# Kernel optimization log

Hardware: AMD Instinct MI355X
Metric: run time of the kernel (lower is better)

The kernel has to match this reference:

```python
import jax, jax.numpy as jnp
import numpy as np

EPSILON = 0.05
MAX_ITER = 50
ALPHA = 6.0
THRESHOLD = 0.25
SCALE = 0.02  # keeps OT costs near THRESHOLD so the gate is not saturated


def setup_inputs() -> dict:
    key = jax.random.key(0)
    k1, k2 = jax.random.split(key)
    B, E, D, P = 8192, 8, 512, 32
    tokens = jax.random.normal(k1, (B, E, D), dtype=jnp.float32) * SCALE
    prototypes = jax.random.normal(k2, (E, P, D), dtype=jnp.float32) * SCALE
    return {"tokens": tokens, "prototypes": prototypes, "full_index": 0}


def _sinkhorn_log(cost, epsilon, max_iter):
    # cost: [..., n_source, n_target]; batched log-domain Sinkhorn, fixed iterations
    ns, nt = cost.shape[-2], cost.shape[-1]
    log_mu = jnp.full(cost.shape[:-1], -float(np.log(ns)), dtype=cost.dtype)
    log_nu = jnp.full(cost.shape[:-2] + (nt,), -float(np.log(nt)), dtype=cost.dtype)
    log_k = -cost / epsilon

    def step(carry, _):
        log_u, log_v = carry
        log_u = log_mu - jax.scipy.special.logsumexp(log_k + log_v[..., None, :], axis=-1)
        log_v = log_nu - jax.scipy.special.logsumexp(log_k + log_u[..., :, None], axis=-2)
        return (log_u, log_v), None

    (log_u, log_v), _ = jax.lax.scan(
        step, (jnp.zeros_like(log_mu), jnp.zeros_like(log_nu)), None, length=max_iter
    )
    return jnp.exp(log_k + log_u[..., :, None] + log_v[..., None, :])


def reference(tokens, prototypes, full_index):
    # tokens: [B, E, D], prototypes: [E, P, D]
    B, E, D = tokens.shape
    anchor = tokens[:, full_index, :]                                   # [B, D]
    source = jnp.stack(
        [tokens, jnp.broadcast_to(anchor[:, None, :], tokens.shape)], axis=2
    )                                                                   # [B, E, 2, D]
    # squared euclidean cdist: ||s||^2 - 2 s.p + ||p||^2
    s2 = jnp.sum(source * source, axis=-1)                              # [B, E, 2]
    p2 = jnp.sum(prototypes * prototypes, axis=-1)                      # [E, P]
    cross = jnp.einsum('besd,epd->besp', source, prototypes)            # [B, E, 2, P]
    cost = jnp.maximum(s2[..., None] - 2.0 * cross + p2[None, :, None, :], 0.0)
    transport = _sinkhorn_log(cost, EPSILON, MAX_ITER)                  # [B, E, 2, P]
    ot_cost = jnp.sum(transport * cost, axis=(-1, -2))                  # [B, E]
    validity = jax.nn.sigmoid(-ALPHA * (ot_cost - THRESHOLD))[..., None]  # [B, E, 1]
    # the full_index expert always passes with validity 1 and zero cost
    is_full = jnp.arange(E) == full_index                               # [E]
    ot_cost = jnp.where(is_full[None, :], 0.0, ot_cost)
    validity = jnp.where(is_full[None, :, None], 1.0, validity)
    return validity, ot_cost
```

## Files before the change

kernel.cpp:

```cpp
#include <hip/hip_runtime.h>
#include <hip/hip_bf16.h>


#define EXP2F(x) __builtin_amdgcn_exp2f(x)
#define LOG2F(x) __builtin_amdgcn_logf(x)
#define RCPF(x)  __builtin_amdgcn_rcpf(x)

typedef __bf16 bf16x8 __attribute__((ext_vector_type(8)));
typedef float  f32x4  __attribute__((ext_vector_type(4)));

#define BDIM 8192
#define EDIM 8
#define DDIM 512
#define PDIM 32
#define BPB  64
#define MROWS 128
#define NTHR 256
#define CSTRIDE 36
#define C_SCALE 28.853900817779268f
#define LOG2E   1.4426950408889634f

__device__ __forceinline__ bf16x8 cvt2(float4 a, float4 b) {
  bf16x8 r;
  r[0] = (__bf16)a.x; r[1] = (__bf16)a.y; r[2] = (__bf16)a.z; r[3] = (__bf16)a.w;
  r[4] = (__bf16)b.x; r[5] = (__bf16)b.y; r[6] = (__bf16)b.z; r[7] = (__bf16)b.w;
  return r;
}

__global__ __launch_bounds__(NTHR, 3)
void ot_noise_gate_kernel(const float* __restrict__ tokens,
                          const float* __restrict__ protos,
                          const int*   __restrict__ fullIndexPtr,
                          float*       __restrict__ out) {
  const int fi    = fullIndexPtr[0];
  const int e     = blockIdx.x & (EDIM - 1);
  const int chunk = blockIdx.x >> 3;
  const int b0    = chunk * BPB;
  float* outVal = out;
  float* outOt  = out + BDIM * EDIM;

  if (e == fi) {
    int t = threadIdx.x;
    if (t < BPB) {
      int b = b0 + t;
      outVal[b * EDIM + e] = 1.0f;
      outOt [b * EDIM + e] = 0.0f;
    }
    return;
  }

  __shared__ __align__(16) __bf16 sB[64 * PDIM * 8];
  __shared__ __align__(16) unsigned char sACraw[MROWS * CSTRIDE * 4];
  __shared__ float sNorm[MROWS];
  __shared__ float sPNp[8][33];
  __shared__ float sPN[PDIM];
  __bf16* sA = (__bf16*)sACraw;
  float*  sC = (float*)sACraw;

  const int t   = threadIdx.x;
  const int l   = t & 63;
  const int w   = t >> 6;
  const int fr  = l & 15;
  const int q4  = l >> 4;

  const int row = t >> 1;
  const int h   = t & 1;
  const float4* rowPtr = (const float4*)(tokens +
      ((size_t)(b0 + (row & 63)) * EDIM + ((row < 64) ? e : fi)) * DDIM);

  float4 pf[8];
  #pragma unroll
  for (int i2 = 0; i2 < 8; ++i2) pf[i2] = rowPtr[h * 8 + i2];

  {
    const float4* pG4 = (const float4*)(protos + (size_t)e * PDIM * DDIM);
    const int p  = t & 31;
    const int oh = t >> 5;
    float pnp = 0.f;
    #pragma unroll
    for (int pass = 0; pass < 8; ++pass) {
      int oct = oh * 8 + pass;
      float4 a = pG4[p * 128 + oct * 2];
      float4 b = pG4[p * 128 + oct * 2 + 1];
      pnp += a.x*a.x + a.y*a.y + a.z*a.z + a.w*a.w
           + b.x*b.x + b.y*b.y + b.z*b.z + b.w*b.w;
      *(bf16x8*)&sB[(oct * PDIM + p) * 8] = cvt2(a, b);
    }
    sPNp[oh][p] = pnp;
  }
  __syncthreads();
  if (t < PDIM) {
    float s = 0.f;
    #pragma unroll
    for (int o = 0; o < 8; ++o) s += sPNp[o][t];
    sPN[t] = s;
  }

  f32x4 acc[2][2];
  #pragma unroll
  for (int mt = 0; mt < 2; ++mt)
    #pragma unroll
    for (int nt = 0; nt < 2; ++nt)
      acc[mt][nt] = (f32x4){0.f, 0.f, 0.f, 0.f};
  float ss = 0.f;

  for (int kc = 0; kc < 8; ++kc) {
    #pragma unroll
    for (int ii = 0; ii < 4; ++ii) {
      float4 a = pf[2 * ii], b = pf[2 * ii + 1];
      ss += a.x*a.x + a.y*a.y + a.z*a.z + a.w*a.w
          + b.x*b.x + b.y*b.y + b.z*b.z + b.w*b.w;
      *(bf16x8*)&sA[((h * 4 + ii) * MROWS + row) * 8] = cvt2(a, b);
    }
    __syncthreads();

    if (kc < 7) {
      #pragma unroll
      for (int i2 = 0; i2 < 8; ++i2)
        pf[i2] = rowPtr[(kc + 1) * 16 + h * 8 + i2];
    }

    #pragma unroll
    for (int ks = 0; ks < 2; ++ks) {
      bf16x8 bf0 = *(const bf16x8*)&sB[((kc * 8 + ks * 4 + q4) * PDIM + fr) * 8];
      bf16x8 bf1 = *(const bf16x8*)&sB[((kc * 8 + ks * 4 + q4) * PDIM + 16 + fr) * 8];
      #pragma unroll
      for (int mt = 0; mt < 2; ++mt) {
        bf16x8 af = *(const bf16x8*)&sA[((ks * 4 + q4) * MROWS + w * 32 + mt * 16 + fr) * 8];
        acc[mt][0] = __builtin_amdgcn_mfma_f32_16x16x32_bf16(af, bf0, acc[mt][0], 0, 0, 0);
        acc[mt][1] = __builtin_amdgcn_mfma_f32_16x16x32_bf16(af, bf1, acc[mt][1], 0, 0, 0);
      }
    }
    __syncthreads();
  }

  ss += __shfl_xor(ss, 1);
  if (h == 0) sNorm[row] = ss;
  __syncthreads();

  {
    float pp0 = sPN[fr], pp1 = sPN[16 + fr];
    #pragma unroll
    for (int mt = 0; mt < 2; ++mt)
      #pragma unroll
      for (int reg = 0; reg < 4; ++reg) {
        int r2 = w * 32 + mt * 16 + q4 * 4 + reg;
        float nrm = sNorm[r2];
        sC[r2 * CSTRIDE + fr]      = fmaxf(nrm - 2.f * acc[mt][0][reg] + pp0, 0.f);
        sC[r2 * CSTRIDE + 16 + fr] = fmaxf(nrm - 2.f * acc[mt][1][reg] + pp1, 0.f);
      }
  }
  __syncthreads();

  const int i  = t >> 2;
  const int q2 = t & 3;
  float c0[8], c1[8];
  {
    const float4* r0 = (const float4*)&sC[i * CSTRIDE + q2 * 8];
    const float4* r1 = (const float4*)&sC[(64 + i) * CSTRIDE + q2 * 8];
    #pragma unroll
    for (int r = 0; r < 2; ++r) {
      float4 a = r0[r];
      float4 b = r1[r];
      c0[4*r] = a.x; c0[4*r+1] = a.y; c0[4*r+2] = a.z; c0[4*r+3] = a.w;
      c1[4*r] = b.x; c1[4*r+1] = b.y; c1[4*r+2] = b.z; c1[4*r+3] = b.w;
    }
  }

  float W[8], dc[8];
  float sum0 = 0.f, mA = -1e30f, mB = -1e30f;
  #pragma unroll
  for (int r = 0; r < 8; ++r) {
    float ka = -c0[r] * C_SCALE, kb = -c1[r] * C_SCALE;
    dc[r] = c1[r] - c0[r];
    sum0 += c0[r];
    mA = fmaxf(mA, ka);
    mB = fmaxf(mB, kb);
  }
  mA = fmaxf(mA, __shfl_xor(mA, 1)); mA = fmaxf(mA, __shfl_xor(mA, 2));
  mB = fmaxf(mB, __shfl_xor(mB, 1)); mB = fmaxf(mB, __shfl_xor(mB, 2));
  float sa = 0.f, sb = 0.f;
  #pragma unroll
  for (int r = 0; r < 8; ++r) {
    float ka = -c0[r] * C_SCALE, kb = -c1[r] * C_SCALE;
    sa += EXP2F(ka - mA);
    sb += EXP2F(kb - mB);
    W[r] = EXP2F(C_SCALE * dc[r]);
  }
  sa += __shfl_xor(sa, 1); sa += __shfl_xor(sa, 2);
  sb += __shfl_xor(sb, 1); sb += __shfl_xor(sb, 2);
  sum0 += __shfl_xor(sum0, 1); sum0 += __shfl_xor(sum0, 2);
  float delta = (mB + LOG2F(sb)) - (mA + LOG2F(sa));

  for (int it = 0; it < 49; ++it) {
    float s = EXP2F(delta);
    float T = 0.f;
    #pragma unroll
    for (int r = 0; r < 8; ++r)
      T += RCPF(__builtin_fmaf(W[r], s, 1.0f));
    T += __shfl_xor(T, 1);
    T += __shfl_xor(T, 2);
    delta += LOG2F(T) - LOG2F(32.0f - T);
  }

  float s = EXP2F(delta), sv = 0.f;
  #pragma unroll
  for (int r = 0; r < 8; ++r)
    sv += RCPF(__builtin_fmaf(W[r], s, 1.0f)) * dc[r];
  sv += __shfl_xor(sv, 1);
  sv += __shfl_xor(sv, 2);
  if (q2 == 0) {
    int b = b0 + i;
    float ot  = (sum0 + sv) * 0.03125f;
    float val = RCPF(1.0f + EXP2F(LOG2E * 6.0f * (ot - 0.25f)));
    outVal[b * EDIM + e] = val;
    outOt [b * EDIM + e] = ot;
  }
}

extern "C" void kernel_launch(void* const* d_in, const int* in_sizes, int n_in,
                              void* d_out, int out_size, void* d_ws, size_t ws_size,
                              hipStream_t stream) {
  const float* tokens = (const float*)d_in[0];
  const float* protos = (const float*)d_in[1];
  const int*   fidx   = (const int*)d_in[2];
  float* out = (float*)d_out;

  dim3 grid((BDIM / BPB) * EDIM);
  ot_noise_gate_kernel<<<grid, NTHR, 0, stream>>>(tokens, protos, fidx, out);
}
```

Measured before the change: 218.5 us.

## Restructure to per-wave 8-row tiles with register-fed MFMA and early Sinkhorn exit

Each block now handles 32 batch rows instead of 64, and each wave owns 8 rows (plus their anchor rows). Token data goes straight from global memory into the MFMA A operand in registers, which removes the shared-memory A staging and the block-wide barriers in the K loop. Cost rows are regrouped per wave in a small shared buffer, and the Sinkhorn reduction spreads across 8 lanes per row using a 3-step shuffle. A wave-level ballot ends the fixed 49 iterations early once every update falls below a tolerance, which can change results slightly compared with running all iterations.

Result: faster. 208.3 us (-4.7%).

```diff
diff --git a/kernel.cpp b/kernel.cpp
--- a/kernel.cpp
+++ b/kernel.cpp
@@ -13,10 +13,8 @@
 #define EDIM 8
 #define DDIM 512
 #define PDIM 32
-#define BPB  64
-#define MROWS 128
+#define BPB  32
 #define NTHR 256
-#define CSTRIDE 36
 #define C_SCALE 28.853900817779268f
 #define LOG2E   1.4426950408889634f
 
@@ -34,8 +32,7 @@
                           float*       __restrict__ out) {
   const int fi    = fullIndexPtr[0];
   const int e     = blockIdx.x & (EDIM - 1);
-  const int chunk = blockIdx.x >> 3;
-  const int b0    = chunk * BPB;
+  const int b0    = (blockIdx.x >> 3) * BPB;
   float* outVal = out;
   float* outOt  = out + BDIM * EDIM;
 
@@ -50,27 +47,21 @@
   }
 
   __shared__ __align__(16) __bf16 sB[64 * PDIM * 8];
-  __shared__ __align__(16) unsigned char sACraw[MROWS * CSTRIDE * 4];
-  __shared__ float sNorm[MROWS];
-  __shared__ float sPNp[8][33];
-  __shared__ float sPN[PDIM];
-  __bf16* sA = (__bf16*)sACraw;
-  float*  sC = (float*)sACraw;
-
-  const int t   = threadIdx.x;
-  const int l   = t & 63;
-  const int w   = t >> 6;
-  const int fr  = l & 15;
-  const int q4  = l >> 4;
-
-  const int row = t >> 1;
-  const int h   = t & 1;
-  const float4* rowPtr = (const float4*)(tokens +
-      ((size_t)(b0 + (row & 63)) * EDIM + ((row < 64) ? e : fi)) * DDIM);
-
-  float4 pf[8];
-  #pragma unroll
-  for (int i2 = 0; i2 < 8; ++i2) pf[i2] = rowPtr[h * 8 + i2];
+  __shared__ float sPNp[8][PDIM];
+  __shared__ __align__(16) float sCw[4][16][36];
+
+  const int t  = threadIdx.x;
+  const int l  = t & 63;
+  const int w  = t >> 6;
+  const int fr = l & 15;
+  const int q4 = l >> 4;
+
+  const int bRow = b0 + 8 * w + (fr & 7);
+  const int eSel = (fr < 8) ? e : fi;
+  const float4* rp4 = (const float4*)(tokens + ((size_t)bRow * EDIM + eSel) * DDIM);
+
+  float4 ca0 = rp4[q4 * 2];
+  float4 ca1 = rp4[q4 * 2 + 1];
 
   {
     const float4* pG4 = (const float4*)(protos + (size_t)e * PDIM * DDIM);
@@ -89,128 +80,109 @@
     sPNp[oh][p] = pnp;
   }
   __syncthreads();
-  if (t < PDIM) {
-    float s = 0.f;
-    #pragma unroll
-    for (int o = 0; o < 8; ++o) s += sPNp[o][t];
-    sPN[t] = s;
-  }
-
-  f32x4 acc[2][2];
-  #pragma unroll
-  for (int mt = 0; mt < 2; ++mt)
-    #pragma unroll
-    for (int nt = 0; nt < 2; ++nt)
-      acc[mt][nt] = (f32x4){0.f, 0.f, 0.f, 0.f};
+
+  f32x4 acc0 = (f32x4){0.f, 0.f, 0.f, 0.f};
+  f32x4 acc1 = (f32x4){0.f, 0.f, 0.f, 0.f};
   float ss = 0.f;
 
-  for (int kc = 0; kc < 8; ++kc) {
-    #pragma unroll
-    for (int ii = 0; ii < 4; ++ii) {
-      float4 a = pf[2 * ii], b = pf[2 * ii + 1];
-      ss += a.x*a.x + a.y*a.y + a.z*a.z + a.w*a.w
-          + b.x*b.x + b.y*b.y + b.z*b.z + b.w*b.w;
-      *(bf16x8*)&sA[((h * 4 + ii) * MROWS + row) * 8] = cvt2(a, b);
+  #pragma unroll
+  for (int kc = 0; kc < 16; ++kc) {
+    float4 na0, na1;
+    if (kc < 15) {
+      na0 = rp4[(kc + 1) * 8 + q4 * 2];
+      na1 = rp4[(kc + 1) * 8 + q4 * 2 + 1];
     }
-    __syncthreads();
-
-    if (kc < 7) {
-      #pragma unroll
-      for (int i2 = 0; i2 < 8; ++i2)
-        pf[i2] = rowPtr[(kc + 1) * 16 + h * 8 + i2];
-    }
-
-    #pragma unroll
-    for (int ks = 0; ks < 2; ++ks) {
-      bf16x8 bf0 = *(const bf16x8*)&sB[((kc * 8 + ks * 4 + q4) * PDIM + fr) * 8];
-      bf16x8 bf1 = *(const bf16x8*)&sB[((kc * 8 + ks * 4 + q4) * PDIM + 16 + fr) * 8];
-      #pragma unroll
-      for (int mt = 0; mt < 2; ++mt) {
-        bf16x8 af = *(const bf16x8*)&sA[((ks * 4 + q4) * MROWS + w * 32 + mt * 16 + fr) * 8];
-        acc[mt][0] = __builtin_amdgcn_mfma_f32_16x16x32_bf16(af, bf0, acc[mt][0], 0, 0, 0);
-        acc[mt][1] = __builtin_amdgcn_mfma_f32_16x16x32_bf16(af, bf1, acc[mt][1], 0, 0, 0);
-      }
-    }
-    __syncthreads();
-  }
-
-  ss += __shfl_xor(ss, 1);
-  if (h == 0) sNorm[row] = ss;
-  __syncthreads();
-
+    ss += ca0.x*ca0.x + ca0.y*ca0.y + ca0.z*ca0.z + ca0.w*ca0.w
+        + ca1.x*ca1.x + ca1.y*ca1.y + ca1.z*ca1.z + ca1.w*ca1.w;
+    bf16x8 aF  = cvt2(ca0, ca1);
+    bf16x8 bF0 = *(const bf16x8*)&sB[((kc * 4 + q4) * PDIM + fr) * 8];
+    bf16x8 bF1 = *(const bf16x8*)&sB[((kc * 4 + q4) * PDIM + 16 + fr) * 8];
+    acc0 = __builtin_amdgcn_mfma_f32_16x16x32_bf16(aF, bF0, acc0, 0, 0, 0);
+    acc1 = __builtin_amdgcn_mfma_f32_16x16x32_bf16(aF, bF1, acc1, 0, 0, 0);
+    ca0 = na0; ca1 = na1;
+  }
+
+  ss += __shfl_xor(ss, 16);
+  ss += __shfl_xor(ss, 32);
+  float pn_a = 0.f, pn_b = 0.f;
+  #pragma unroll
+  for (int o = 0; o < 8; ++o) {
+    pn_a += sPNp[o][fr];
+    pn_b += sPNp[o][16 + fr];
+  }
+
+  #pragma unroll
+  for (int reg = 0; reg < 4; ++reg) {
+    int row = q4 * 4 + reg;
+    float nrm = __shfl(ss, row);
+    sCw[w][row][fr]      = fmaxf(nrm - 2.f * acc0[reg] + pn_a, 0.f);
+    sCw[w][row][16 + fr] = fmaxf(nrm - 2.f * acc1[reg] + pn_b, 0.f);
+  }
+
+  const int i = l & 7;
+  const int s = l >> 3;
+  float c0[4], c1[4];
   {
-    float pp0 = sPN[fr], pp1 = sPN[16 + fr];
-    #pragma unroll
-    for (int mt = 0; mt < 2; ++mt)
-      #pragma unroll
-      for (int reg = 0; reg < 4; ++reg) {
-        int r2 = w * 32 + mt * 16 + q4 * 4 + reg;
-        float nrm = sNorm[r2];
-        sC[r2 * CSTRIDE + fr]      = fmaxf(nrm - 2.f * acc[mt][0][reg] + pp0, 0.f);
-        sC[r2 * CSTRIDE + 16 + fr] = fmaxf(nrm - 2.f * acc[mt][1][reg] + pp1, 0.f);
-      }
-  }
-  __syncthreads();
-
-  const int i  = t >> 2;
-  const int q2 = t & 3;
-  float c0[8], c1[8];
-  {
-    const float4* r0 = (const float4*)&sC[i * CSTRIDE + q2 * 8];
-    const float4* r1 = (const float4*)&sC[(64 + i) * CSTRIDE + q2 * 8];
-    #pragma unroll
-    for (int r = 0; r < 2; ++r) {
-      float4 a = r0[r];
-      float4 b = r1[r];
-      c0[4*r] = a.x; c0[4*r+1] = a.y; c0[4*r+2] = a.z; c0[4*r+3] = a.w;
-      c1[4*r] = b.x; c1[4*r+1] = b.y; c1[4*r+2] = b.z; c1[4*r+3] = b.w;
-    }
-  }
-
-  float W[8], dc[8];
+    float4 v0 = *(const float4*)&sCw[w][i][4 * s];
+    float4 v1 = *(const float4*)&sCw[w][8 + i][4 * s];
+    c0[0] = v0.x; c0[1] = v0.y; c0[2] = v0.z; c0[3] = v0.w;
+    c1[0] = v1.x; c1[1] = v1.y; c1[2] = v1.z; c1[3] = v1.w;
+  }
+
+  float W[4], dc[4];
   float sum0 = 0.f, mA = -1e30f, mB = -1e30f;
   #pragma unroll
-  for (int r = 0; r < 8; ++r) {
+  for (int r = 0; r < 4; ++r) {
     float ka = -c0[r] * C_SCALE, kb = -c1[r] * C_SCALE;
     dc[r] = c1[r] - c0[r];
     sum0 += c0[r];
     mA = fmaxf(mA, ka);
     mB = fmaxf(mB, kb);
   }
-  mA = fmaxf(mA, __shfl_xor(mA, 1)); mA = fmaxf(mA, __shfl_xor(mA, 2));
-  mB = fmaxf(mB, __shfl_xor(mB, 1)); mB = fmaxf(mB, __shfl_xor(mB, 2));
+  mA = fmaxf(mA, __shfl_xor(mA, 8));
+  mA = fmaxf(mA, __shfl_xor(mA, 16));
+  mA = fmaxf(mA, __shfl_xor(mA, 32));
+  mB = fmaxf(mB, __shfl_xor(mB, 8));
+  mB = fmaxf(mB, __shfl_xor(mB, 16));
+  mB = fmaxf(mB, __shfl_xor(mB, 32));
   float sa = 0.f, sb = 0.f;
   #pragma unroll
-  for (int r = 0; r < 8; ++r) {
+  for (int r = 0; r < 4; ++r) {
     float ka = -c0[r] * C_SCALE, kb = -c1[r] * C_SCALE;
     sa += EXP2F(ka - mA);
     sb += EXP2F(kb - mB);
     W[r] = EXP2F(C_SCALE * dc[r]);
   }
-  sa += __shfl_xor(sa, 1); sa += __shfl_xor(sa, 2);
-  sb += __shfl_xor(sb, 1); sb += __shfl_xor(sb, 2);
-  sum0 += __shfl_xor(sum0, 1); sum0 += __shfl_xor(sum0, 2);
+  sa += __shfl_xor(sa, 8);  sa += __shfl_xor(sa, 16);  sa += __shfl_xor(sa, 32);
+  sb += __shfl_xor(sb, 8);  sb += __shfl_xor(sb, 16);  sb += __shfl_xor(sb, 32);
+  sum0 += __shfl_xor(sum0, 8);
+  sum0 += __shfl_xor(sum0, 16);
+  sum0 += __shfl_xor(sum0, 32);
   float delta = (mB + LOG2F(sb)) - (mA + LOG2F(sa));
 
   for (int it = 0; it < 49; ++it) {
-    float s = EXP2F(delta);
+    float s2 = EXP2F(delta);
     float T = 0.f;
     #pragma unroll
-    for (int r = 0; r < 8; ++r)
-      T += RCPF(__builtin_fmaf(W[r], s, 1.0f));
-    T += __shfl_xor(T, 1);
-    T += __shfl_xor(T, 2);
-    delta += LOG2F(T) - LOG2F(32.0f - T);
-  }
-
-  float s = EXP2F(delta), sv = 0.f;
-  #pragma unroll
-  for (int r = 0; r < 8; ++r)
-    sv += RCPF(__builtin_fmaf(W[r], s, 1.0f)) * dc[r];
-  sv += __shfl_xor(sv, 1);
-  sv += __shfl_xor(sv, 2);
-  if (q2 == 0) {
-    int b = b0 + i;
+    for (int r = 0; r < 4; ++r)
+      T += RCPF(__builtin_fmaf(W[r], s2, 1.0f));
+    T += __shfl_xor(T, 8);
+    T += __shfl_xor(T, 16);
+    T += __shfl_xor(T, 32);
+    float upd = LOG2F(T) - LOG2F(32.0f - T);
+    delta += upd;
+    if (__ballot(fabsf(upd) > 5e-7f) == 0ull) break;
+  }
+
+  float s2 = EXP2F(delta), sv = 0.f;
+  #pragma unroll
+  for (int r = 0; r < 4; ++r)
+    sv += RCPF(__builtin_fmaf(W[r], s2, 1.0f)) * dc[r];
+  sv += __shfl_xor(sv, 8);
+  sv += __shfl_xor(sv, 16);
+  sv += __shfl_xor(sv, 32);
+  if (s == 0) {
+    int b = b0 + 8 * w + i;
     float ot  = (sum0 + sv) * 0.03125f;
     float val = RCPF(1.0f + EXP2F(LOG2E * 6.0f * (ot - 0.25f)));
     outVal[b * EDIM + e] = val;
```
